# Kernel tuning notes

Measured on AMD Instinct MI355X. Metric: run time of the kernel, lower is better.

The kernel has to match this reference:

```python
import jax, jax.numpy as jnp
import numpy as np


def setup_inputs() -> dict:
    key = jax.random.key(0)
    kq, kk, kv = jax.random.split(key, 3)
    B, H, S, D = 2, 8, 4096, 64
    return {
        "query": jax.random.normal(kq, (B, H, S, D), dtype=jnp.float32),
        "key": jax.random.normal(kk, (B, H, S, D), dtype=jnp.float32),
        "value": jax.random.normal(kv, (B, H, S, D), dtype=jnp.float32),
    }


def reference(query, key, value):
    # NOTE: the torch source overwrites sqrt(d) with d, so the divisor is D, not sqrt(D).
    d = query.shape[-1]
    # score: [B, H, S_q, S_k]
    score = jnp.einsum("bhqd,bhkd->bhqk", query, key) / d
    relu = jax.nn.relu(score)  # no softmax / row normalization
    out = jnp.einsum("bhqk,bhkd->bhqd", relu, value)
    return out
```

## Files before the change

kernel.cpp:

```cpp
#include <hip/hip_runtime.h>
#include <hip/hip_bf16.h>
#include <stdint.h>


#define NH 16
#define SEQ 4096
#define DD 64
#define HE (SEQ*DD)
#define HB (HE*2)
#define Q16_OFF 0
#define K16_OFF (NH*HB)
#define V16_OFF (2*NH*HB)
#define WS_NEED (3*NH*HB)

typedef __attribute__((ext_vector_type(8)))  short    bf16x8;
typedef __attribute__((ext_vector_type(16))) float    f32x16;
typedef __attribute__((ext_vector_type(4)))  uint32_t u32x4;

__device__ inline uint32_t f2bf1(float f) {
  return (uint32_t)__builtin_bit_cast(unsigned short, __float2bfloat16(f));
}
__device__ inline uint32_t pack2bf(float a, float b) {
  return f2bf1(a) | (f2bf1(b) << 16);
}
__device__ inline uint32_t cvtpk(float lo, float hi) {
  uint32_t r;
  asm("v_cvt_pk_bf16_f32 %0, %1, %2" : "=v"(r) : "v"(lo), "v"(hi));
  return r;
}
__device__ inline uint32_t relu2(uint32_t w) {
  uint32_t r;
  asm("v_pk_max_f16 %0, %1, 0" : "=v"(r) : "v"(w));
  return r;
}

__global__ __launch_bounds__(256) void prepass_kernel(const float* __restrict__ Q,
                                                      const float* __restrict__ K,
                                                      const float* __restrict__ V,
                                                      char* __restrict__ ws) {
  __shared__ float vt[64*65];
  int bx = blockIdx.x, tid = threadIdx.x;
  if (bx < 2048) {
    int head = bx >> 7, qg = bx & 127;
    int r31 = tid & 31, c = tid >> 5;
    const float4* s = (const float4*)(Q + (size_t)head*HE + ((size_t)(qg*32 + r31))*64 + c*8);
    float4 a = s[0], b = s[1];
    const float sc = 1.0f/64.0f;
    u32x4 o;
    o.x = pack2bf(a.x*sc, a.y*sc);
    o.y = pack2bf(a.z*sc, a.w*sc);
    o.z = pack2bf(b.x*sc, b.y*sc);
    o.w = pack2bf(b.z*sc, b.w*sc);
    char* tb = ws + Q16_OFF + (size_t)head*HB;
    *(u32x4*)(tb + ((qg*4 + (c >> 1))*1024) + ((c & 1)*32 + r31)*16) = o;
  } else if (bx < 3072) {
    int tile = bx - 2048;
    int head = tile >> 6, t = tile & 63;
    int r = tid >> 2, c0 = (tid & 3) * 16;
    const float4* s4 = (const float4*)(K + (size_t)head*HE + ((size_t)(t*64 + r))*64 + c0);
    float4 f0 = s4[0], f1 = s4[1], f2 = s4[2], f3 = s4[3];
    u32x4 c_lo, c_hi;
    c_lo.x = pack2bf(f0.x, f0.y); c_lo.y = pack2bf(f0.z, f0.w);
    c_lo.z = pack2bf(f1.x, f1.y); c_lo.w = pack2bf(f1.z, f1.w);
    c_hi.x = pack2bf(f2.x, f2.y); c_hi.y = pack2bf(f2.z, f2.w);
    c_hi.z = pack2bf(f3.x, f3.y); c_hi.w = pack2bf(f3.z, f3.w);
    char* tb = ws + K16_OFF + ((size_t)head*64 + t)*8192;
    char* chunk = tb + ((r >> 5)*4 + (tid & 3))*1024 + (r & 31)*16;
    *(u32x4*)(chunk)       = c_lo;
    *(u32x4*)(chunk + 512) = c_hi;
  } else {
    int tile = bx - 3072;
    int head = tile >> 6, t = tile & 63;
    int k = tid >> 2, c0 = (tid & 3)*16;
    const float4* s4 = (const float4*)(V + (size_t)head*HE + ((size_t)(t*64 + k))*64 + c0);
    float4 f0 = s4[0], f1 = s4[1], f2 = s4[2], f3 = s4[3];
    float tmp[16] = {f0.x,f0.y,f0.z,f0.w, f1.x,f1.y,f1.z,f1.w,
                     f2.x,f2.y,f2.z,f2.w, f3.x,f3.y,f3.z,f3.w};
    #pragma unroll
    for (int j = 0; j < 16; ++j) vt[k*65 + c0 + j] = tmp[j];
    __syncthreads();
    int d = tid >> 2, k0 = (tid & 3)*16;
    float v2[16];
    #pragma unroll
    for (int j = 0; j < 16; ++j) v2[j] = vt[(k0 + j)*65 + d];
    u32x4 c_lo, c_hi;
    c_lo.x = pack2bf(v2[0],  v2[1]);  c_lo.y = pack2bf(v2[2],  v2[3]);
    c_lo.z = pack2bf(v2[4],  v2[5]);  c_lo.w = pack2bf(v2[6],  v2[7]);
    c_hi.x = pack2bf(v2[8],  v2[9]);  c_hi.y = pack2bf(v2[10], v2[11]);
    c_hi.z = pack2bf(v2[12], v2[13]); c_hi.w = pack2bf(v2[14], v2[15]);
    char* tb = ws + V16_OFF + ((size_t)head*64 + t)*8192;
    char* chunk = tb + ((d >> 5)*4 + (tid & 3))*1024 + (d & 31)*16;
    *(u32x4*)(chunk)       = c_lo;
    *(u32x4*)(chunk + 512) = c_hi;
  }
}

__global__ __launch_bounds__(256, 2) void attn_kernel(const char* __restrict__ ws,
                                                      float* __restrict__ out) {
  __shared__ float red[128*64];
  int bid = blockIdx.x;
  int bx = (bid & 7) * 64 + (bid >> 3);
  int head = bx >> 5, qblk = bx & 31;
  int tid = threadIdx.x;
  int lane = tid & 63, w = tid >> 6;
  int l31 = lane & 31, h = lane >> 5;
  int g  = w >> 1;
  int wg = w & 1;

  const char* q16   = ws + Q16_OFF + (size_t)head*HB;
  const char* kbase = ws + K16_OFF + (size_t)head*HB + (size_t)g*32*8192;
  const char* vbase = ws + V16_OFF + (size_t)head*HB + (size_t)g*32*8192;

  int qg0 = qblk*4 + wg*2;
  bf16x8 qf[2][4];
  #pragma unroll
  for (int m = 0; m < 2; ++m)
    #pragma unroll
    for (int t = 0; t < 4; ++t)
      qf[m][t] = *(const bf16x8*)(q16 + ((size_t)((qg0 + m)*4 + t))*1024 + lane*16);

  f32x16 kZero;
  #pragma unroll
  for (int i = 0; i < 16; ++i) kZero[i] = 0.f;

  f32x16 o[2][2];
  #pragma unroll
  for (int m = 0; m < 2; ++m)
    #pragma unroll
    for (int nd = 0; nd < 2; ++nd)
      #pragma unroll
      for (int i = 0; i < 16; ++i) o[m][nd][i] = 0.f;

  bf16x8 kf[2][4], vf[2][4];

  auto loadK = [&](int kt) {
    const char* kp = kbase + (size_t)kt*8192;
    #pragma unroll
    for (int i = 0; i < 8; ++i)
      kf[i >> 2][i & 3] = *(const bf16x8*)(kp + i*1024 + lane*16);
  };
  auto loadV = [&](int kt) {
    const char* vp = vbase + (size_t)kt*8192;
    #pragma unroll
    for (int i = 0; i < 8; ++i)
      vf[i >> 2][i & 3] = *(const bf16x8*)(vp + i*1024 + lane*16);
  };

  loadK(0);
  #pragma unroll 1
  for (int kt = 0; kt < 32; ++kt) {
    loadV(kt);

    f32x16 st[2][2];
    #pragma unroll
    for (int n = 0; n < 2; ++n) {
      __builtin_amdgcn_s_setprio(1);
      #pragma unroll
      for (int m = 0; m < 2; ++m) {
        f32x16 acc = __builtin_amdgcn_mfma_f32_32x32x16_bf16(kf[n][0], qf[m][0], kZero, 0, 0, 0);
        #pragma unroll
        for (int t = 1; t < 4; ++t)
          acc = __builtin_amdgcn_mfma_f32_32x32x16_bf16(kf[n][t], qf[m][t], acc, 0, 0, 0);
        st[m][n] = acc;
      }
      __builtin_amdgcn_s_setprio(0);
    }

    loadK((kt + 1) & 31);

    bf16x8 pa[2][4];
    #pragma unroll
    for (int m = 0; m < 2; ++m)
      #pragma unroll
      for (int n = 0; n < 2; ++n)
        #pragma unroll
        for (int kn = 0; kn < 2; ++kn) {
          uint32_t w0 = cvtpk(st[m][n][kn*8+0], st[m][n][kn*8+1]);
          uint32_t w1 = cvtpk(st[m][n][kn*8+2], st[m][n][kn*8+3]);
          uint32_t w2 = cvtpk(st[m][n][kn*8+4], st[m][n][kn*8+5]);
          uint32_t w3 = cvtpk(st[m][n][kn*8+6], st[m][n][kn*8+7]);
          asm("v_permlane32_swap_b32 %0, %1" : "+v"(w0), "+v"(w2));
          asm("v_permlane32_swap_b32 %0, %1" : "+v"(w1), "+v"(w3));
          union { uint32_t u[4]; bf16x8 v; } pk;
          pk.u[0] = relu2(w0);
          pk.u[1] = relu2(w1);
          pk.u[2] = relu2(w2);
          pk.u[3] = relu2(w3);
          pa[m][n*2 + kn] = pk.v;
        }

    __builtin_amdgcn_s_setprio(1);
    #pragma unroll
    for (int m = 0; m < 2; ++m)
      #pragma unroll
      for (int nd = 0; nd < 2; ++nd)
        #pragma unroll
        for (int ks = 0; ks < 4; ++ks)
          o[m][nd] = __builtin_amdgcn_mfma_f32_32x32x16_bf16(pa[m][ks], vf[nd][ks], o[m][nd], 0, 0, 0);
    __builtin_amdgcn_s_setprio(0);

    if ((kt & 7) == 7) __builtin_amdgcn_s_barrier();
  }

  __syncthreads();
  if (g == 1) {
    #pragma unroll
    for (int m = 0; m < 2; ++m)
      #pragma unroll
      for (int nd = 0; nd < 2; ++nd)
        #pragma unroll
        for (int r = 0; r < 16; ++r) {
          int ql = wg*64 + m*32 + (r & 3) + 8*(r >> 2) + 4*h;
          red[ql*64 + nd*32 + l31] = o[m][nd][r];
        }
  }
  __syncthreads();
  if (g == 0) {
    float* outh = out + (size_t)head*HE;
    #pragma unroll
    for (int m = 0; m < 2; ++m)
      #pragma unroll
      for (int nd = 0; nd < 2; ++nd)
        #pragma unroll
        for (int r = 0; r < 16; ++r) {
          int ql = wg*64 + m*32 + (r & 3) + 8*(r >> 2) + 4*h;
          float v = o[m][nd][r] + red[ql*64 + nd*32 + l31];
          outh[(size_t)(qblk*128 + ql)*64 + nd*32 + l31] = v;
        }
  }
}

extern "C" void kernel_launch(void* const* d_in, const int* in_sizes, int n_in,
                              void* d_out, int out_size, void* d_ws, size_t ws_size,
                              hipStream_t stream) {
  if (n_in < 3 || ws_size < (size_t)WS_NEED) return;
  const float* Q = (const float*)d_in[0];
  const float* K = (const float*)d_in[1];
  const float* V = (const float*)d_in[2];
  float* out = (float*)d_out;
  char* ws = (char*)d_ws;
  hipLaunchKernelGGL(prepass_kernel, dim3(4096), dim3(256), 0, stream, Q, K, V, ws);
  hipLaunchKernelGGL(attn_kernel,    dim3(512),  dim3(256), 0, stream, ws, out);
}
```

Baseline: 80.24 us.

## Stage K tiles through LDS with async global_load_lds triple buffering

K tiles are no longer loaded into registers separately by each wave. Each wave now issues half of a tile's chunks through global_load_lds into a three-slot LDS ring that it shares with its partner wave. Both waves then read the full tile from LDS, which removes the duplicated global K reads and prefetches two tiles ahead. The cost is a workgroup barrier plus a vmcnt wait on every iteration, and more LDS use (48KB), which could limit overlap between waves.

```diff
diff --git a/kernel.cpp b/kernel.cpp
--- a/kernel.cpp
+++ b/kernel.cpp
@@ -97,7 +97,7 @@
 
 __global__ __launch_bounds__(256, 2) void attn_kernel(const char* __restrict__ ws,
                                                       float* __restrict__ out) {
-  __shared__ float red[128*64];
+  __shared__ __align__(16) char lds[6*8192];
   int bid = blockIdx.x;
   int bx = (bid & 7) * 64 + (bid >> 3);
   int head = bx >> 5, qblk = bx & 31;
@@ -131,13 +131,18 @@
       #pragma unroll
       for (int i = 0; i < 16; ++i) o[m][nd][i] = 0.f;
 
-  bf16x8 kf[2][4], vf[2][4];
-
-  auto loadK = [&](int kt) {
-    const char* kp = kbase + (size_t)kt*8192;
-    #pragma unroll
-    for (int i = 0; i < 8; ++i)
-      kf[i >> 2][i & 3] = *(const bf16x8*)(kp + i*1024 + lane*16);
+  bf16x8 vf[2][4];
+
+  auto stageK = [&](int kt) {
+    const char* ktile = kbase + (size_t)kt*8192;
+    char* lk = lds + (size_t)(g*3 + kt % 3)*8192;
+    #pragma unroll
+    for (int c = 0; c < 4; ++c) {
+      int off = (wg*4 + c)*1024;
+      __builtin_amdgcn_global_load_lds(
+          (const __attribute__((address_space(1))) void*)(ktile + off + lane*16),
+          (__attribute__((address_space(3))) void*)(lk + off), 16, 0, 0);
+    }
   };
   auto loadV = [&](int kt) {
     const char* vp = vbase + (size_t)kt*8192;
@@ -146,10 +151,22 @@
       vf[i >> 2][i & 3] = *(const bf16x8*)(vp + i*1024 + lane*16);
   };
 
-  loadK(0);
+  stageK(0);
+  stageK(1);
   #pragma unroll 1
   for (int kt = 0; kt < 32; ++kt) {
+    if (kt >= 30) asm volatile("s_waitcnt vmcnt(0)" ::: "memory");
+    else          asm volatile("s_waitcnt vmcnt(4)" ::: "memory");
+    __builtin_amdgcn_s_barrier();
+
     loadV(kt);
+    if (kt + 2 < 32) stageK(kt + 2);
+
+    const char* lk = lds + (size_t)(g*3 + kt % 3)*8192;
+    bf16x8 kf[2][4];
+    #pragma unroll
+    for (int i = 0; i < 8; ++i)
+      kf[i >> 2][i & 3] = *(const bf16x8*)(lk + i*1024 + lane*16);
 
     f32x16 st[2][2];
     #pragma unroll
@@ -165,8 +182,6 @@
       }
       __builtin_amdgcn_s_setprio(0);
     }
-
-    loadK((kt + 1) & 31);
 
     bf16x8 pa[2][4];
     #pragma unroll
@@ -198,11 +213,10 @@
         for (int ks = 0; ks < 4; ++ks)
           o[m][nd] = __builtin_amdgcn_mfma_f32_32x32x16_bf16(pa[m][ks], vf[nd][ks], o[m][nd], 0, 0, 0);
     __builtin_amdgcn_s_setprio(0);
-
-    if ((kt & 7) == 7) __builtin_amdgcn_s_barrier();
   }
 
   __syncthreads();
+  float* red = (float*)lds;
   if (g == 1) {
     #pragma unroll
     for (int m = 0; m < 2; ++m)
```

Measured after the change: 82.27 us. 2.5% more time.
